# Kernel tuning notes

Hardware: AMD Instinct MI355X
Metric: run time of the kernel (lower is better)

The kernel has to match this reference:

```python
import jax, jax.numpy as jnp
import numpy as np
from jax import lax

D_MODEL = 1024
D_INNER = 2 * D_MODEL          # expand=2
D_STATE = 16
D_CONV = 4
DT_RANK = 64                   # ceil(1024/16)
DT_MIN = 0.001
DT_MAX = 0.1
BATCH = 4
SEQ = 2048


def setup_inputs() -> dict:
    key = jax.random.key(0)
    ks = jax.random.split(key, 8)
    s = lambda fan_in: 1.0 / np.sqrt(fan_in)
    x = jax.random.normal(ks[0], (BATCH, SEQ, D_MODEL), dtype=jnp.float32)
    # Linear weights stored as (in, out) so y = x @ W
    W_in = jax.random.uniform(ks[1], (D_MODEL, 2 * D_INNER), jnp.float32, -s(D_MODEL), s(D_MODEL))
    conv_w = jax.random.uniform(ks[2], (D_INNER, 1, D_CONV), jnp.float32, -s(D_CONV), s(D_CONV))
    conv_b = jax.random.uniform(ks[3], (D_INNER,), jnp.float32, -s(D_CONV), s(D_CONV))
    W_x = jax.random.uniform(ks[4], (D_INNER, DT_RANK + 2 * D_STATE), jnp.float32, -s(D_INNER), s(D_INNER))
    W_dt = jax.random.uniform(ks[5], (DT_RANK, D_INNER), jnp.float32, -s(DT_RANK), s(DT_RANK))
    b_dt = jax.random.uniform(ks[6], (D_INNER,), jnp.float32, -s(DT_RANK), s(DT_RANK))
    # A = arange(1..d_state) repeated over d_inner; store log(A)
    A_log = jnp.log(jnp.broadcast_to(jnp.arange(1, D_STATE + 1, dtype=jnp.float32), (D_INNER, D_STATE)))
    D_param = jnp.ones((D_INNER,), dtype=jnp.float32)
    W_out = jax.random.uniform(ks[7], (D_INNER, D_MODEL), jnp.float32, -s(D_INNER), s(D_INNER))
    return {"x": x, "W_in": W_in, "conv_w": conv_w, "conv_b": conv_b,
            "W_x": W_x, "W_dt": W_dt, "b_dt": b_dt, "A_log": A_log,
            "D_param": D_param, "W_out": W_out}


def reference(x, W_in, conv_w, conv_b, W_x, W_dt, b_dt, A_log, D_param, W_out):
    # in_proj + split
    xz = x @ W_in                                   # (B, S, 2*d_inner)
    x_branch, z_branch = jnp.split(xz, 2, axis=-1)  # each (B, S, d_inner)

    # causal depthwise conv1d (torch pads d_conv-1 both sides then slices [:seq])
    xc = jnp.pad(x_branch.transpose(0, 2, 1), ((0, 0), (0, 0), (D_CONV - 1, 0)))
    xc = lax.conv_general_dilated(xc, conv_w, (1,), 'VALID',
                                  dimension_numbers=('NCH', 'OIH', 'NCH'),
                                  feature_group_count=D_INNER)
    xc = xc + conv_b[None, :, None]
    x_conv = jax.nn.silu(xc.transpose(0, 2, 1))     # (B, S, d_inner)

    # input-dependent dt, B, C
    x_dbl = x_conv @ W_x                            # (B, S, dt_rank + 2*d_state)
    dt_low = x_dbl[..., :DT_RANK]
    Bm = x_dbl[..., DT_RANK:DT_RANK + D_STATE]      # (B, S, d_state)
    Cm = x_dbl[..., DT_RANK + D_STATE:]             # (B, S, d_state)
    dt = jax.nn.sigmoid(dt_low @ W_dt + b_dt) * (DT_MAX - DT_MIN) + DT_MIN
    dt = jnp.maximum(dt, 1e-4)                      # (B, S, d_inner)

    A = -jnp.exp(A_log)                             # (d_inner, d_state)

    # selective scan over time (n_substeps = 1)
    def step(h, inp):
        dt_t, B_t, C_t, x_t = inp                   # (B,di), (B,ds), (B,ds), (B,di)
        dA = jnp.exp(dt_t[:, :, None] * A[None])    # (B, di, ds)
        h = dA * h + (dt_t * x_t)[:, :, None] * B_t[:, None, :]
        y_t = jnp.sum(h * C_t[:, None, :], axis=-1) # (B, di)
        return h, y_t

    h0 = jnp.zeros((x.shape[0], D_INNER, D_STATE), dtype=x.dtype)
    _, ys = lax.scan(step, h0,
                     (dt.swapaxes(0, 1), Bm.swapaxes(0, 1),
                      Cm.swapaxes(0, 1), x_conv.swapaxes(0, 1)))
    y = ys.swapaxes(0, 1)                           # (B, S, d_inner)

    y = y + x_conv * D_param
    y = y * jax.nn.silu(z_branch)
    return y @ W_out                                # (B, S, d_model)
```

## Files before the change

kernel.cpp:

```cpp
#include <hip/hip_runtime.h>

typedef unsigned short u16;
typedef unsigned int u32;
typedef __attribute__((ext_vector_type(8))) short short8;
typedef __attribute__((ext_vector_type(4))) float f32x4;

#define NBATCH 4
#define NSEQ   2048
#define DMODEL 1024
#define DINNER 2048
#define DSTATE 16
#define DTRANK 64
#define ROWS   (NBATCH*NSEQ)
#define NCH    64
#define CLEN   32

__device__ __forceinline__ float b2f(u16 u){ union{u32 i; float f;} v; v.i=((u32)u)<<16; return v.f; }
__device__ __forceinline__ u16 f2b(float f){ union{float f; u32 i;} v; v.f=f; u32 i=v.i; return (u16)((i + 0x7FFFu + ((i>>16)&1u))>>16); }
__device__ __forceinline__ float sigmoidf_(float x){ return 1.0f/(1.0f+__expf(-x)); }

__global__ __launch_bounds__(256) void prep(const u16* __restrict__ x,
    const u16* __restrict__ Win, const u16* __restrict__ convw,
    const u16* __restrict__ Wx, const u16* __restrict__ Wdt,
    const u16* __restrict__ Alog, const u16* __restrict__ Wout,
    const u16* __restrict__ v0, const u16* __restrict__ v1, const u16* __restrict__ v2,
    int* __restrict__ meta){
  __shared__ int vote;
  __shared__ int mxbits;
  const int tid = threadIdx.x;
  const u16* V[3] = {v0, v1, v2};

  const u16* ptrs[6] = {x, Win, convw, Wx, Wdt, Wout};
  const float bounds[6] = {8.f, 0.045f, 0.6f, 0.035f, 0.15f, 0.035f};
  const int slots[6] = {0, 1, 2, 4, 5, 9};
  for (int q = 0; q < 6; q++){
    if (tid == 0) vote = 1;
    __syncthreads();
    int bad = 0;
    for (int i = tid; i < 2048; i += 256){
      float v = fabsf(b2f(ptrs[q][i]));
      if (!(v <= bounds[q])) bad = 1;
    }
    if (bad) atomicAnd(&vote, 0);
    __syncthreads();
    if (tid == 0) meta[slots[q]] = vote;
    __syncthreads();
  }
  if (tid == 0){ u16 u = Alog[1]; meta[7] = (u == 0x3F31 || u == 0x3F32) ? 1 : 0; }

  int iD = -1, fD = 1;
  for (int k = 0; k < 3; k++){
    if (V[k][0] == 0x3F80 && V[k][1] == 0x3F80){ iD = k; fD = 1; }
    else if (V[k][0] == 0 && V[k][1] == 0x3F80 && V[k][2] == 0){ iD = k; fD = 0; }
  }
  if (iD < 0){ iD = 2; fD = 1; }
  int oo[2], no = 0;
  for (int k = 0; k < 3; k++) if (k != iD) oo[no++] = k;
  int fo[2]; float mo[2];
  for (int q = 0; q < 2; q++){
    if (tid == 0) vote = 1;
    __syncthreads();
    int bad = 0;
    for (int i = tid; i < 2048; i += 256){
      float v = fabsf(b2f(V[oo[q]][i]));
      if (!(v <= 0.6f)) bad = 1;
    }
    if (bad) atomicAnd(&vote, 0);
    __syncthreads();
    fo[q] = vote;
    if (tid == 0) mxbits = 0;
    __syncthreads();
    float m = 0.f;
    for (int i = tid; i < 2048; i += 256){
      float v = fabsf(fo[q] ? b2f(V[oo[q]][i]) : ((const float*)V[oo[q]])[i]);
      m = fmaxf(m, v);
    }
    atomicMax(&mxbits, __float_as_int(m));
    __syncthreads();
    mo[q] = __int_as_float(mxbits);
    __syncthreads();
  }
  if (tid == 0){
    int a = (mo[0] > 0.25f) ? 0 : 1;
    meta[10] = oo[a];     meta[3] = fo[a];
    meta[11] = oo[1-a];   meta[6] = fo[1-a];
    meta[12] = iD;        meta[8] = fD;
  }
}

__global__ __launch_bounds__(256) void cvt_bf16(const void* __restrict__ in,
                                                u16* __restrict__ out, long n,
                                                const int* __restrict__ meta, int slot){
  long i = (long)blockIdx.x*256 + threadIdx.x;
  if (i >= n) return;
  if (meta[slot]) out[i] = ((const u16*)in)[i];
  else            out[i] = f2b(((const float*)in)[i]);
}

__global__ __launch_bounds__(256) void cvt_trio(const void* __restrict__ v0,
                                                const void* __restrict__ v1,
                                                const void* __restrict__ v2,
                                                const int* __restrict__ meta,
                                                u16* __restrict__ cbc,
                                                u16* __restrict__ bdtc,
                                                u16* __restrict__ dpc){
  int i = blockIdx.x*256 + threadIdx.x;
  int which = i >> 11, d = i & 2047;
  const void* V[3] = {v0, v1, v2};
  int src, fl; u16* dst;
  if (which == 0){ src = meta[10]; fl = meta[3]; dst = cbc; }
  else if (which == 1){ src = meta[11]; fl = meta[6]; dst = bdtc; }
  else { src = meta[12]; fl = meta[8]; dst = dpc; }
  dst[d] = fl ? ((const u16*)V[src])[d] : f2b(((const float*)V[src])[d]);
}

__global__ __launch_bounds__(256) void transpose_pad(const void* __restrict__ inv,
                                                     u16* __restrict__ out,
                                                     int K, int N, int Nout,
                                                     const int* __restrict__ meta, int slot){
  __shared__ u16 t[32][33];
  const int f = meta[slot];
  const u16*   ib = (const u16*)inv;
  const float* iff = (const float*)inv;
  int k0 = blockIdx.x*32, n0 = blockIdx.y*32;
  int tx = threadIdx.x & 31, ty = threadIdx.x >> 5;
  #pragma unroll
  for (int i=0;i<32;i+=8){
    int k = k0+ty+i, n = n0+tx;
    u16 v = 0;
    if (k<K && n<N) v = f ? ib[(long)k*N+n] : f2b(iff[(long)k*N+n]);
    t[ty+i][tx] = v;
  }
  __syncthreads();
  #pragma unroll
  for (int i=0;i<32;i+=8){
    int n = n0+ty+i, k = k0+tx;
    if (n<Nout && k<K) out[(long)n*K+k] = t[tx][ty+i];
  }
}

template<int MODE>
__global__ __launch_bounds__(256) void gemm_bt(
    const u16* __restrict__ A, int lda,
    const u16* __restrict__ Bt, int K,
    u16* __restrict__ C0, u16* __restrict__ C1, int ldc,
    const u16* __restrict__ bias, float* __restrict__ Cf)
{
  __shared__ u16 sa[128*64];
  __shared__ u16 sb[128*64];
  const int tid = threadIdx.x;
  const int lane = tid & 63;
  const int wave = tid >> 6;
  const int wm = (wave >> 1) * 64;
  const int wn = (wave & 1) * 64;
  const int lane15 = lane & 15;
  const int quad = lane >> 4;
  const long rowBase = (long)blockIdx.y * 128;
  const long colBase = (long)blockIdx.x * 128;

  f32x4 acc[4][4];
  #pragma unroll
  for (int i=0;i<4;i++)
    #pragma unroll
    for (int j=0;j<4;j++)
      #pragma unroll
      for (int r=0;r<4;r++) acc[i][j][r]=0.0f;

  const int e  = tid*8;
  const int r0 = e >> 6;
  const int c0 = e & 63;

  for (int kb=0; kb<K; kb+=64) {
    #pragma unroll
    for (int i=0;i<4;i++){
      const u16* ga = A + (rowBase + r0 + i*32)*lda + kb + c0;
      __builtin_amdgcn_global_load_lds((const __attribute__((address_space(1))) void*)ga,
                                       (__attribute__((address_space(3))) void*)&sa[e + i*2048],
                                       16, 0, 0);
    }
    #pragma unroll
    for (int i=0;i<4;i++){
      const u16* gb = Bt + (colBase + r0 + i*32)*(long)K + kb + c0;
      __builtin_amdgcn_global_load_lds((const __attribute__((address_space(1))) void*)gb,
                                       (__attribute__((address_space(3))) void*)&sb[e + i*2048],
                                       16, 0, 0);
    }
    __syncthreads();
    #pragma unroll
    for (int ko=0; ko<2; ko++){
      const int kk = ko*32 + quad*8;
      short8 af[4], bfr[4];
      #pragma unroll
      for (int i=0;i<4;i++) af[i]  = *(const short8*)&sa[(wm + i*16 + lane15)*64 + kk];
      #pragma unroll
      for (int j=0;j<4;j++) bfr[j] = *(const short8*)&sb[(wn + j*16 + lane15)*64 + kk];
      #pragma unroll
      for (int i=0;i<4;i++)
        #pragma unroll
        for (int j=0;j<4;j++)
          acc[i][j] = __builtin_amdgcn_mfma_f32_16x16x32_bf16(af[i], bfr[j], acc[i][j], 0, 0, 0);
    }
    __syncthreads();
  }

  #pragma unroll
  for (int i=0;i<4;i++){
    #pragma unroll
    for (int j=0;j<4;j++){
      long row = rowBase + wm + i*16 + quad*4;
      long col = colBase + wn + j*16 + lane15;
      #pragma unroll
      for (int r=0;r<4;r++){
        float v = acc[i][j][r];
        long rr = row + r;
        if (MODE == 0) {
          C0[rr*ldc + col] = f2b(v);
        } else if (MODE == 2) {
          float t  = sigmoidf_(v + b2f(bias[col]));
          float dv = fmaxf(t*0.099f + 0.001f, 1e-4f);
          C0[rr*ldc + col] = f2b(dv);
        } else if (MODE == 3) {
          Cf[rr*ldc + col] = v;
        }
      }
    }
  }
}

template<int MODE>
__global__ __launch_bounds__(512, 2) void gemm256(
    const u16* __restrict__ A, int lda,
    const u16* __restrict__ Bt, int K,
    u16* __restrict__ C0, u16* __restrict__ C1, int ldc,
    float* __restrict__ Cf)
{
  __shared__ u16 sa[2*16384];
  __shared__ u16 sb[2*16384];
  const int tid  = threadIdx.x;
  const int lane = tid & 63;
  const int wm   = (tid >> 6) >> 2;
  const int wn   = (tid >> 6) & 3;
  const int lane15 = lane & 15;
  const int quad   = lane >> 4;

  const int nwg  = gridDim.x * gridDim.y;
  const int orig = blockIdx.y * gridDim.x + blockIdx.x;
  const int swz  = (orig & 7) * (nwg >> 3) + (orig >> 3);
  const int bx   = swz % gridDim.x;
  const int by   = swz / gridDim.x;
  const long rowBase = (long)by * 256;
  const long colBase = (long)bx * 256;

  const int xorv = (lane15 & 7) << 3;
  const int k0   = (quad*8) ^ xorv;
  const int k1   = (32 + quad*8) ^ xorv;
  const int aBase = (wm*128 + lane15) * 64;
  const int bBase = (wn*64  + lane15) * 64;

  const int scol = ((tid & 7) ^ ((tid >> 3) & 7)) << 3;
  const int arow = tid >> 3;
  const int bsub = ((tid >> 8) & 1)*64 + ((tid & 255) >> 3);
  const int bdst = (tid & 7) * 8;

  f32x4 acc[8][4];
  #pragma unroll
  for (int i=0;i<8;i++)
    #pragma unroll
    for (int j=0;j<4;j++)
      #pragma unroll
      for (int r=0;r<4;r++) acc[i][j][r]=0.0f;

  const int nt = K >> 6;

  auto stageA = [&](int buf, int rs, int kb){
    const u16* g = A + (rowBase + rs + arow)*(long)lda + kb + scol;
    __builtin_amdgcn_global_load_lds((const __attribute__((address_space(1))) void*)g,
        (__attribute__((address_space(3))) void*)&sa[buf*16384 + rs*64 + tid*8], 16, 0, 0);
  };
  auto stageB = [&](int buf, int cq, int part, int kb){
    const int row = part*128 + cq*32 + bsub;
    const u16* g = Bt + (colBase + row)*(long)K + kb + scol;
    __builtin_amdgcn_global_load_lds((const __attribute__((address_space(1))) void*)g,
        (__attribute__((address_space(3))) void*)&sb[buf*16384 + row*64 + bdst], 16, 0, 0);
  };

  stageA(0,   0, 0); stageA(0, 128, 0);
  stageB(0, 0, 0, 0); stageB(0, 0, 1, 0);
  stageA(0,  64, 0); stageA(0, 192, 0);
  stageB(0, 1, 0, 0); stageB(0, 1, 1, 0);
  asm volatile("s_waitcnt vmcnt(4)\n\ts_barrier" ::: "memory");

  for (int t = 0; t < nt; ++t){
    const int cur = t & 1, nb = cur ^ 1;
    const int kb2 = (t+1) << 6;
    const bool pf = (t+1 < nt);
    const u16* sA = &sa[cur*16384];
    const u16* sB = &sb[cur*16384];
    short8 a0[4][2], a1[4][2], b0[2][2], b1[2][2];

    #pragma unroll
    for (int i=0;i<4;i++){
      a0[i][0] = *(const short8*)&sA[aBase + i*1024 + k0];
      a0[i][1] = *(const short8*)&sA[aBase + i*1024 + k1];
    }
    #pragma unroll
    for (int j=0;j<2;j++){
      b0[j][0] = *(const short8*)&sB[bBase + j*1024 + k0];
      b0[j][1] = *(const short8*)&sB[bBase + j*1024 + k1];
    }
    if (pf){ stageA(nb, 0, kb2); stageA(nb, 128, kb2); }
    __builtin_amdgcn_s_setprio(1);
    #pragma unroll
    for (int s=0;s<2;s++)
      #pragma unroll
      for (int i=0;i<4;i++)
        #pragma unroll
        for (int j=0;j<2;j++)
          acc[i][j] = __builtin_amdgcn_mfma_f32_16x16x32_bf16(a0[i][s], b0[j][s], acc[i][j], 0, 0, 0);
    __builtin_amdgcn_s_setprio(0);
    asm volatile("s_waitcnt vmcnt(4)\n\ts_barrier" ::: "memory");

    #pragma unroll
    for (int i=0;i<4;i++){
      a1[i][0] = *(const short8*)&sA[aBase + 4096 + i*1024 + k0];
      a1[i][1] = *(const short8*)&sA[aBase + 4096 + i*1024 + k1];
    }
    if (pf){ stageB(nb, 0, 0, kb2); stageB(nb, 0, 1, kb2); }
    __builtin_amdgcn_s_setprio(1);
    #pragma unroll
    for (int s=0;s<2;s++)
      #pragma unroll
      for (int i=0;i<4;i++)
        #pragma unroll
        for (int j=0;j<2;j++)
          acc[4+i][j] = __builtin_amdgcn_mfma_f32_16x16x32_bf16(a1[i][s], b0[j][s], acc[4+i][j], 0, 0, 0);
    __builtin_amdgcn_s_setprio(0);
    asm volatile("s_waitcnt vmcnt(4)\n\ts_barrier" ::: "memory");

    #pragma unroll
    for (int j=0;j<2;j++){
      b1[j][0] = *(const short8*)&sB[bBase + 2048 + j*1024 + k0];
      b1[j][1] = *(const short8*)&sB[bBase + 2048 + j*1024 + k1];
    }
    if (pf){ stageA(nb, 64, kb2); stageA(nb, 192, kb2); }
    __builtin_amdgcn_s_setprio(1);
    #pragma unroll
    for (int s=0;s<2;s++)
      #pragma unroll
      for (int i=0;i<4;i++)
        #pragma unroll
        for (int j=0;j<2;j++)
          acc[i][2+j] = __builtin_amdgcn_mfma_f32_16x16x32_bf16(a0[i][s], b1[j][s], acc[i][2+j], 0, 0, 0);
    __builtin_amdgcn_s_setprio(0);
    asm volatile("s_barrier" ::: "memory");

    if (pf){ stageB(nb, 1, 0, kb2); stageB(nb, 1, 1, kb2); }
    __builtin_amdgcn_s_setprio(1);
    #pragma unroll
    for (int s=0;s<2;s++)
      #pragma unroll
      for (int i=0;i<4;i++)
        #pragma unroll
        for (int j=0;j<2;j++)
          acc[4+i][2+j] = __builtin_amdgcn_mfma_f32_16x16x32_bf16(a1[i][s], b1[j][s], acc[4+i][2+j], 0, 0, 0);
    __builtin_amdgcn_s_setprio(0);
    asm volatile("s_waitcnt vmcnt(4)\n\ts_barrier" ::: "memory");
  }

  #pragma unroll
  for (int i=0;i<8;i++){
    const long row = rowBase + wm*128 + i*16 + quad*4;
    #pragma unroll
    for (int j=0;j<4;j++){
      const long col = colBase + wn*64 + j*16 + lane15;
      #pragma unroll
      for (int r=0;r<4;r++){
        const float v = acc[i][j][r];
        const long rr = row + r;
        if (MODE == 1){
          if (col < 2048) C0[rr*2048 + col] = f2b(v);
          else            C1[rr*2048 + (col-2048)] = f2b(v);
        } else {
          Cf[rr*ldc + col] = v;
        }
      }
    }
  }
}

__global__ __launch_bounds__(256) void conv_silu(const u16* __restrict__ xb,
                                                 const u16* __restrict__ w,
                                                 const u16* __restrict__ bias,
                                                 u16* __restrict__ xc){
  long idx8 = ((long)blockIdx.x*256 + threadIdx.x) * 8;
  int d = (int)(idx8 & (DINNER-1));
  int s = (int)((idx8 >> 11) & (NSEQ-1));
  int b = (int)(idx8 >> 22);

  short8 bv = *(const short8*)(bias + d);
  short8 wv0 = *(const short8*)(w + d*4);
  short8 wv1 = *(const short8*)(w + d*4 + 8);
  short8 wv2 = *(const short8*)(w + d*4 + 16);
  short8 wv3 = *(const short8*)(w + d*4 + 24);
  u16 wl[32];
  #pragma unroll
  for (int q=0;q<8;q++){ wl[q] = ((u16*)&wv0)[q]; wl[8+q] = ((u16*)&wv1)[q];
                         wl[16+q] = ((u16*)&wv2)[q]; wl[24+q] = ((u16*)&wv3)[q]; }

  float acc[8];
  #pragma unroll
  for (int l=0;l<8;l++) acc[l] = b2f(((u16*)&bv)[l]);

  #pragma unroll
  for (int j=0;j<4;j++){
    int t = s - 3 + j;
    if (t >= 0){
      short8 xv = *(const short8*)(xb + ((long)(b*NSEQ + t))*DINNER + d);
      #pragma unroll
      for (int l=0;l<8;l++)
        acc[l] += b2f(((u16*)&xv)[l]) * b2f(wl[l*4 + j]);
    }
  }
  short8 ov;
  #pragma unroll
  for (int l=0;l<8;l++){ float y = acc[l]*sigmoidf_(acc[l]); ((u16*)&ov)[l] = f2b(y); }
  *(short8*)(xc + idx8) = ov;
}

__global__ __launch_bounds__(256) void scan_pass1(const u16* __restrict__ dt,
                                                  const u16* __restrict__ xc,
                                                  const u16* __restrict__ xdbl,
                                                  const u16* __restrict__ Alog,
                                                  float* __restrict__ hend,
                                                  float* __restrict__ sumdt){
  int d = blockIdx.x*256 + threadIdx.x;
  int c = blockIdx.y;
  int b = blockIdx.z;
  __shared__ float sB[CLEN][DSTATE];
  for (int i=threadIdx.x; i<CLEN*DSTATE; i+=256){
    int t = i >> 4, s = i & 15;
    sB[t][s] = b2f(xdbl[((long)(b*NSEQ + c*CLEN + t))*128 + DTRANK + s]);
  }
  float Acf[DSTATE];
  bool fast = true;
  #pragma unroll
  for (int s=0;s<DSTATE;s++){
    Acf[s] = -__expf(b2f(Alog[d*DSTATE + s]));
    fast = fast && (fabsf(Acf[s] + (float)(s+1)) < 0.03f*(float)(s+1));
  }
  __syncthreads();

  float h[DSTATE];
  #pragma unroll
  for (int s=0;s<DSTATE;s++) h[s] = 0.0f;
  float sd = 0.0f;
  long base = ((long)(b*NSEQ + c*CLEN))*DINNER + d;
  float dtv = b2f(dt[base]);
  float xv  = b2f(xc[base]);
  if (fast){
    for (int t=0;t<CLEN;t++){
      long nxt = base + (long)((t+1<CLEN)?(t+1):t)*DINNER;
      float dtn = b2f(dt[nxt]);
      float xn  = b2f(xc[nxt]);
      float B[DSTATE];
      *(f32x4*)&B[0]  = *(const f32x4*)&sB[t][0];
      *(f32x4*)&B[4]  = *(const f32x4*)&sB[t][4];
      *(f32x4*)&B[8]  = *(const f32x4*)&sB[t][8];
      *(f32x4*)&B[12] = *(const f32x4*)&sB[t][12];
      float u = dtv*xv;
      sd += dtv;
      float e1 = __expf(-dtv);
      float p = e1;
      #pragma unroll
      for (int s=0;s<DSTATE;s++){
        h[s] = fmaf(p, h[s], u*B[s]);
        p *= e1;
      }
      dtv = dtn; xv = xn;
    }
  } else {
    for (int t=0;t<CLEN;t++){
      long nxt = base + (long)((t+1<CLEN)?(t+1):t)*DINNER;
      float dtn = b2f(dt[nxt]);
      float xn  = b2f(xc[nxt]);
      float B[DSTATE];
      *(f32x4*)&B[0]  = *(const f32x4*)&sB[t][0];
      *(f32x4*)&B[4]  = *(const f32x4*)&sB[t][4];
      *(f32x4*)&B[8]  = *(const f32x4*)&sB[t][8];
      *(f32x4*)&B[12] = *(const f32x4*)&sB[t][12];
      float u = dtv*xv;
      sd += dtv;
      #pragma unroll
      for (int s=0;s<DSTATE;s++){
        float dA = __expf(dtv * Acf[s]);
        h[s] = fmaf(dA, h[s], u*B[s]);
      }
      dtv = dtn; xv = xn;
    }
  }
  long hidx = ((long)(b*DINNER + d)*NCH + c)*DSTATE;
  #pragma unroll
  for (int s=0;s<DSTATE;s++) hend[hidx + s] = h[s];
  sumdt[(long)(b*DINNER + d)*NCH + c] = sd;
}

__global__ __launch_bounds__(256) void scan_pass2(float* __restrict__ hend,
                                                  const float* __restrict__ sumdt,
                                                  const u16* __restrict__ Alog){
  long i = (long)blockIdx.x*256 + threadIdx.x;
  int s = (int)(i & 15);
  long bd = i >> 4;
  int d = (int)(bd & (DINNER-1));
  float A = -__expf(b2f(Alog[d*DSTATE + s]));
  float run = 0.0f;
  long base = bd*NCH*DSTATE + s;
  for (int c=0;c<NCH;c++){
    float e = hend[base + (long)c*DSTATE];
    float decay = __expf(A * sumdt[bd*NCH + c]);
    hend[base + (long)c*DSTATE] = run;
    run = run*decay + e;
  }
}

__global__ __launch_bounds__(256) void scan_pass3(const u16* __restrict__ dt,
                                                  u16* __restrict__ xc,
                                                  const u16* __restrict__ zb,
                                                  const u16* __restrict__ xdbl,
                                                  const u16* __restrict__ Alog,
                                                  const u16* __restrict__ Dp,
                                                  const float* __restrict__ hstart){
  int d = blockIdx.x*256 + threadIdx.x;
  int c = blockIdx.y;
  int b = blockIdx.z;
  __shared__ float sB[CLEN][DSTATE];
  __shared__ float sC[CLEN][DSTATE];
  for (int i=threadIdx.x; i<CLEN*DSTATE; i+=256){
    int t = i >> 4, s = i & 15;
    long rb = ((long)(b*NSEQ + c*CLEN + t))*128;
    sB[t][s] = b2f(xdbl[rb + DTRANK + s]);
    sC[t][s] = b2f(xdbl[rb + DTRANK + DSTATE + s]);
  }
  float Acf[DSTATE];
  bool fast = true;
  #pragma unroll
  for (int s=0;s<DSTATE;s++){
    Acf[s] = -__expf(b2f(Alog[d*DSTATE + s]));
    fast = fast && (fabsf(Acf[s] + (float)(s+1)) < 0.03f*(float)(s+1));
  }
  __syncthreads();

  float h[DSTATE];
  long hidx = ((long)(b*DINNER + d)*NCH + c)*DSTATE;
  #pragma unroll
  for (int s=0;s<DSTATE;s++) h[s] = hstart[hidx + s];
  float Dpv = b2f(Dp[d]);
  long base = ((long)(b*NSEQ + c*CLEN))*DINNER + d;
  float dtv = b2f(dt[base]);
  float xv  = b2f(xc[base]);
  float zv  = b2f(zb[base]);
  if (fast){
    for (int t=0;t<CLEN;t++){
      long nxt = base + (long)((t+1<CLEN)?(t+1):t)*DINNER;
      float dtn = b2f(dt[nxt]);
      float xn  = b2f(xc[nxt]);
      float zn  = b2f(zb[nxt]);
      float B[DSTATE], C[DSTATE];
      *(f32x4*)&B[0]  = *(const f32x4*)&sB[t][0];
      *(f32x4*)&B[4]  = *(const f32x4*)&sB[t][4];
      *(f32x4*)&B[8]  = *(const f32x4*)&sB[t][8];
      *(f32x4*)&B[12] = *(const f32x4*)&sB[t][12];
      *(f32x4*)&C[0]  = *(const f32x4*)&sC[t][0];
      *(f32x4*)&C[4]  = *(const f32x4*)&sC[t][4];
      *(f32x4*)&C[8]  = *(const f32x4*)&sC[t][8];
      *(f32x4*)&C[12] = *(const f32x4*)&sC[t][12];
      float u = dtv*xv;
      float e1 = __expf(-dtv);
      float gate = zv*sigmoidf_(zv);
      float p = e1;
      float y = 0.0f;
      #pragma unroll
      for (int s=0;s<DSTATE;s++){
        h[s] = fmaf(p, h[s], u*B[s]);
        y = fmaf(h[s], C[s], y);
        p *= e1;
      }
      y = fmaf(xv, Dpv, y);
      y *= gate;
      xc[base + (long)t*DINNER] = f2b(y);
      dtv = dtn; xv = xn; zv = zn;
    }
  } else {
    for (int t=0;t<CLEN;t++){
      long nxt = base + (long)((t+1<CLEN)?(t+1):t)*DINNER;
      float dtn = b2f(dt[nxt]);
      float xn  = b2f(xc[nxt]);
      float zn  = b2f(zb[nxt]);
      float B[DSTATE], C[DSTATE];
      *(f32x4*)&B[0]  = *(const f32x4*)&sB[t][0];
      *(f32x4*)&B[4]  = *(const f32x4*)&sB[t][4];
      *(f32x4*)&B[8]  = *(const f32x4*)&sB[t][8];
      *(f32x4*)&B[12] = *(const f32x4*)&sB[t][12];
      *(f32x4*)&C[0]  = *(const f32x4*)&sC[t][0];
      *(f32x4*)&C[4]  = *(const f32x4*)&sC[t][4];
      *(f32x4*)&C[8]  = *(const f32x4*)&sC[t][8];
      *(f32x4*)&C[12] = *(const f32x4*)&sC[t][12];
      float u = dtv*xv;
      float gate = zv*sigmoidf_(zv);
      float y = 0.0f;
      #pragma unroll
      for (int s=0;s<DSTATE;s++){
        float dA = __expf(dtv * Acf[s]);
        h[s] = fmaf(dA, h[s], u*B[s]);
        y = fmaf(h[s], C[s], y);
      }
      y = fmaf(xv, Dpv, y);
      y *= gate;
      xc[base + (long)t*DINNER] = f2b(y);
      dtv = dtn; xv = xn; zv = zn;
    }
  }
}

extern "C" void kernel_launch(void* const* d_in, const int* in_sizes, int n_in,
                              void* d_out, int out_size, void* d_ws, size_t ws_size,
                              hipStream_t stream) {
  const void *x=nullptr,*W_in=nullptr,*conv_w=nullptr,*W_x=nullptr,*W_dt=nullptr,
             *A_log=nullptr,*W_out=nullptr;
  const void* v2048[3] = {nullptr,nullptr,nullptr};
  int n2048 = 0;
  for (int i = 0; i < n_in; i++){
    switch (in_sizes[i]){
      case 8388608: x      = d_in[i]; break;
      case 4194304: W_in   = d_in[i]; break;
      case 8192:    conv_w = d_in[i]; break;
      case 196608:  W_x    = d_in[i]; break;
      case 131072:  W_dt   = d_in[i]; break;
      case 32768:   A_log  = d_in[i]; break;
      case 2097152: W_out  = d_in[i]; break;
      case 2048:    if (n2048 < 3) v2048[n2048++] = d_in[i]; break;
      default: break;
    }
  }

  size_t off = 0;
  char* wsb = (char*)d_ws;
  auto take = [&](size_t n){ void* p = wsb + off; off += (n + 255) & ~(size_t)255; return p; };
  u16* Wt_in  = (u16*)take((size_t)4096*1024*2);
  u16* Wt_x   = (u16*)take((size_t)128*2048*2);
  u16* Wt_dt  = (u16*)take((size_t)2048*64*2);
  u16* Wt_out = (u16*)take((size_t)1024*2048*2);
  u16* xb     = (u16*)take((size_t)ROWS*DINNER*2);
  u16* zb     = (u16*)take((size_t)ROWS*DINNER*2);
  u16* xc     = (u16*)take((size_t)ROWS*DINNER*2);
  u16* xdbl   = (u16*)take((size_t)ROWS*128*2);
  char* shr = (char*)take((size_t)ROWS*NCH*DSTATE*4 + (size_t)ROWS*NCH*4 + 4096);
  u16*   xcvt  = (u16*)shr;
  float* hend  = (float*)shr;
  float* sumdt = (float*)(shr + (size_t)ROWS*NCH*DSTATE*4);
  u16* cwc  = (u16*)take(DINNER*4*2);
  u16* cbc  = (u16*)take(DINNER*2);
  u16* bdtc = (u16*)take(DINNER*2);
  u16* alc  = (u16*)take(DINNER*DSTATE*2);
  u16* dpc  = (u16*)take(DINNER*2);
  int* meta = (int*)take(256);
  u16* dtb = xb;

  prep<<<1, 256, 0, stream>>>((const u16*)x, (const u16*)W_in, (const u16*)conv_w,
                              (const u16*)W_x, (const u16*)W_dt, (const u16*)A_log,
                              (const u16*)W_out,
                              (const u16*)v2048[0], (const u16*)v2048[1], (const u16*)v2048[2],
                              meta);

  cvt_bf16<<<(ROWS*DMODEL)/256, 256, 0, stream>>>(x, xcvt, (long)ROWS*DMODEL, meta, 0);
  cvt_bf16<<<32, 256, 0, stream>>>(conv_w, cwc, DINNER*4, meta, 2);
  cvt_bf16<<<128,256, 0, stream>>>(A_log, alc, DINNER*DSTATE, meta, 7);
  cvt_trio<<<24, 256, 0, stream>>>(v2048[0], v2048[1], v2048[2], meta, cbc, bdtc, dpc);

  transpose_pad<<<dim3(32,128), 256, 0, stream>>>(W_in, Wt_in, 1024, 4096, 4096, meta, 1);
  transpose_pad<<<dim3(64,4),   256, 0, stream>>>(W_x,  Wt_x,  2048, 96,   128,  meta, 4);
  transpose_pad<<<dim3(2,64),   256, 0, stream>>>(W_dt, Wt_dt, 64,   2048, 2048, meta, 5);
  transpose_pad<<<dim3(64,32),  256, 0, stream>>>(W_out,Wt_out,2048, 1024, 1024, meta, 9);

  gemm256<1><<<dim3(16,32), 512, 0, stream>>>(xcvt, 1024, Wt_in, 1024, xb, zb, 2048, nullptr);

  conv_silu<<<(ROWS*DINNER)/(256*8), 256, 0, stream>>>(xb, cwc, cbc, xc);

  gemm_bt<0><<<dim3(1,64), 256, 0, stream>>>(xc, 2048, Wt_x, 2048, xdbl, nullptr, 128, nullptr, nullptr);

  gemm_bt<2><<<dim3(16,64), 256, 0, stream>>>(xdbl, 128, Wt_dt, 64, dtb, nullptr, 2048, bdtc, nullptr);

  scan_pass1<<<dim3(8,NCH,NBATCH), 256, 0, stream>>>(dtb, xc, xdbl, alc, hend, sumdt);
  scan_pass2<<<(ROWS*DSTATE)/256, 256, 0, stream>>>(hend, sumdt, alc);
  scan_pass3<<<dim3(8,NCH,NBATCH), 256, 0, stream>>>(dtb, xc, zb, xdbl, alc, dpc, hend);

  gemm_bt<3><<<dim3(8,64), 256, 0, stream>>>(xc, 2048, Wt_out, 2048, nullptr, nullptr, 1024, nullptr, (float*)d_out);
}
```

Measured before the change: 476.4 us.

## Split-K the x_proj GEMM, vectorize x conversion, 4 channels per scan thread

```diff
diff --git a/kernel.cpp b/kernel.cpp
--- a/kernel.cpp
+++ b/kernel.cpp
@@ -3,6 +3,7 @@
 typedef unsigned short u16;
 typedef unsigned int u32;
 typedef __attribute__((ext_vector_type(8))) short short8;
+typedef __attribute__((ext_vector_type(4))) short short4v;
 typedef __attribute__((ext_vector_type(4))) float f32x4;
 
 #define NBATCH 4
@@ -95,6 +96,23 @@
   if (i >= n) return;
   if (meta[slot]) out[i] = ((const u16*)in)[i];
   else            out[i] = f2b(((const float*)in)[i]);
+}
+
+__global__ __launch_bounds__(256) void cvt_x8(const void* __restrict__ in,
+                                              u16* __restrict__ out,
+                                              const int* __restrict__ meta){
+  long i8 = ((long)blockIdx.x*256 + threadIdx.x)*8;
+  if (meta[0]){
+    *(short8*)(out + i8) = *(const short8*)((const u16*)in + i8);
+  } else {
+    const float* f = (const float*)in + i8;
+    f32x4 a = *(const f32x4*)f;
+    f32x4 b = *(const f32x4*)(f+4);
+    short8 o;
+    #pragma unroll
+    for (int j=0;j<4;j++){ ((u16*)&o)[j] = f2b(a[j]); ((u16*)&o)[4+j] = f2b(b[j]); }
+    *(short8*)(out + i8) = o;
+  }
 }
 
 __global__ __launch_bounds__(256) void cvt_trio(const void* __restrict__ v0,
@@ -158,6 +176,14 @@
   const long rowBase = (long)blockIdx.y * 128;
   const long colBase = (long)blockIdx.x * 128;
 
+  int kbeg = 0, kend = K;
+  if (MODE == 4){
+    const int span = K >> 2;
+    kbeg = blockIdx.z * span;
+    kend = kbeg + span;
+    Cf += (long)blockIdx.z * (8192L*128);
+  }
+
   f32x4 acc[4][4];
   #pragma unroll
   for (int i=0;i<4;i++)
@@ -170,7 +196,7 @@
   const int r0 = e >> 6;
   const int c0 = e & 63;
 
-  for (int kb=0; kb<K; kb+=64) {
+  for (int kb=kbeg; kb<kend; kb+=64) {
     #pragma unroll
     for (int i=0;i<4;i++){
       const u16* ga = A + (rowBase + r0 + i*32)*lda + kb + c0;
@@ -219,12 +245,25 @@
           float t  = sigmoidf_(v + b2f(bias[col]));
           float dv = fmaxf(t*0.099f + 0.001f, 1e-4f);
           C0[rr*ldc + col] = f2b(dv);
-        } else if (MODE == 3) {
+        } else if (MODE == 3 || MODE == 4) {
           Cf[rr*ldc + col] = v;
         }
       }
     }
   }
+}
+
+__global__ __launch_bounds__(256) void reduce_xdbl(const float* __restrict__ P,
+                                                   u16* __restrict__ out){
+  const long i4 = ((long)blockIdx.x*256 + threadIdx.x)*4;
+  f32x4 a = *(const f32x4*)(P + i4);
+  f32x4 b = *(const f32x4*)(P + 1048576 + i4);
+  f32x4 c = *(const f32x4*)(P + 2097152 + i4);
+  f32x4 d = *(const f32x4*)(P + 3145728 + i4);
+  short4v o;
+  #pragma unroll
+  for (int j=0;j<4;j++) ((u16*)&o)[j] = f2b(a[j]+b[j]+c[j]+d[j]);
+  *(short4v*)(out + i4) = o;
 }
 
 template<int MODE>
@@ -433,75 +472,97 @@
                                                   const u16* __restrict__ Alog,
                                                   float* __restrict__ hend,
                                                   float* __restrict__ sumdt){
-  int d = blockIdx.x*256 + threadIdx.x;
-  int c = blockIdx.y;
-  int b = blockIdx.z;
+  const int tid = threadIdx.x;
+  const int d0 = blockIdx.x*1024 + tid*4;
+  const int c = blockIdx.y;
+  const int b = blockIdx.z;
   __shared__ float sB[CLEN][DSTATE];
-  for (int i=threadIdx.x; i<CLEN*DSTATE; i+=256){
+  for (int i=tid; i<CLEN*DSTATE; i+=256){
     int t = i >> 4, s = i & 15;
     sB[t][s] = b2f(xdbl[((long)(b*NSEQ + c*CLEN + t))*128 + DTRANK + s]);
   }
-  float Acf[DSTATE];
   bool fast = true;
   #pragma unroll
-  for (int s=0;s<DSTATE;s++){
-    Acf[s] = -__expf(b2f(Alog[d*DSTATE + s]));
-    fast = fast && (fabsf(Acf[s] + (float)(s+1)) < 0.03f*(float)(s+1));
-  }
+  for (int j=0;j<4;j++)
+    #pragma unroll
+    for (int s=0;s<DSTATE;s++){
+      float a = -__expf(b2f(Alog[(d0+j)*DSTATE + s]));
+      fast = fast && (fabsf(a + (float)(s+1)) < 0.03f*(float)(s+1));
+    }
   __syncthreads();
 
-  float h[DSTATE];
-  #pragma unroll
-  for (int s=0;s<DSTATE;s++) h[s] = 0.0f;
-  float sd = 0.0f;
-  long base = ((long)(b*NSEQ + c*CLEN))*DINNER + d;
-  float dtv = b2f(dt[base]);
-  float xv  = b2f(xc[base]);
+  float h[4][DSTATE];
+  #pragma unroll
+  for (int j=0;j<4;j++)
+    #pragma unroll
+    for (int s=0;s<DSTATE;s++) h[j][s] = 0.0f;
+  float sd[4] = {0.f,0.f,0.f,0.f};
+  long base = ((long)(b*NSEQ + c*CLEN))*DINNER + d0;
+  short4v dt4 = *(const short4v*)(dt + base);
+  short4v x4  = *(const short4v*)(xc + base);
   if (fast){
     for (int t=0;t<CLEN;t++){
       long nxt = base + (long)((t+1<CLEN)?(t+1):t)*DINNER;
-      float dtn = b2f(dt[nxt]);
-      float xn  = b2f(xc[nxt]);
+      short4v dtn = *(const short4v*)(dt + nxt);
+      short4v xn  = *(const short4v*)(xc + nxt);
       float B[DSTATE];
       *(f32x4*)&B[0]  = *(const f32x4*)&sB[t][0];
       *(f32x4*)&B[4]  = *(const f32x4*)&sB[t][4];
       *(f32x4*)&B[8]  = *(const f32x4*)&sB[t][8];
       *(f32x4*)&B[12] = *(const f32x4*)&sB[t][12];
-      float u = dtv*xv;
-      sd += dtv;
-      float e1 = __expf(-dtv);
-      float p = e1;
-      #pragma unroll
-      for (int s=0;s<DSTATE;s++){
-        h[s] = fmaf(p, h[s], u*B[s]);
-        p *= e1;
+      #pragma unroll
+      for (int j=0;j<4;j++){
+        float dtv = b2f(((u16*)&dt4)[j]);
+        float xv  = b2f(((u16*)&x4)[j]);
+        float u = dtv*xv;
+        sd[j] += dtv;
+        float e1 = __expf(-dtv);
+        float p = e1;
+        #pragma unroll
+        for (int s=0;s<DSTATE;s++){
+          h[j][s] = fmaf(p, h[j][s], u*B[s]);
+          p *= e1;
+        }
       }
-      dtv = dtn; xv = xn;
+      dt4 = dtn; x4 = xn;
     }
   } else {
+    float Acf[4][DSTATE];
+    #pragma unroll
+    for (int j=0;j<4;j++)
+      #pragma unroll
+      for (int s=0;s<DSTATE;s++) Acf[j][s] = -__expf(b2f(Alog[(d0+j)*DSTATE + s]));
     for (int t=0;t<CLEN;t++){
       long nxt = base + (long)((t+1<CLEN)?(t+1):t)*DINNER;
-      float dtn = b2f(dt[nxt]);
-      float xn  = b2f(xc[nxt]);
+      short4v dtn = *(const short4v*)(dt + nxt);
+      short4v xn  = *(const short4v*)(xc + nxt);
       float B[DSTATE];
       *(f32x4*)&B[0]  = *(const f32x4*)&sB[t][0];
       *(f32x4*)&B[4]  = *(const f32x4*)&sB[t][4];
       *(f32x4*)&B[8]  = *(const f32x4*)&sB[t][8];
       *(f32x4*)&B[12] = *(const f32x4*)&sB[t][12];
-      float u = dtv*xv;
-      sd += dtv;
-      #pragma unroll
-      for (int s=0;s<DSTATE;s++){
-        float dA = __expf(dtv * Acf[s]);
-        h[s] = fmaf(dA, h[s], u*B[s]);
+      #pragma unroll
+      for (int j=0;j<4;j++){
+        float dtv = b2f(((u16*)&dt4)[j]);
+        float xv  = b2f(((u16*)&x4)[j]);
+        float u = dtv*xv;
+        sd[j] += dtv;
+        #pragma unroll
+        for (int s=0;s<DSTATE;s++){
+          float dA = __expf(dtv * Acf[j][s]);
+          h[j][s] = fmaf(dA, h[j][s], u*B[s]);
+        }
       }
-      dtv = dtn; xv = xn;
-    }
-  }
-  long hidx = ((long)(b*DINNER + d)*NCH + c)*DSTATE;
-  #pragma unroll
-  for (int s=0;s<DSTATE;s++) hend[hidx + s] = h[s];
-  sumdt[(long)(b*DINNER + d)*NCH + c] = sd;
+      dt4 = dtn; x4 = xn;
+    }
+  }
+  #pragma unroll
+  for (int j=0;j<4;j++){
+    long hidx = ((long)(b*DINNER + d0 + j)*NCH + c)*DSTATE;
+    #pragma unroll
+    for (int q=0;q<4;q++) *(f32x4*)&hend[hidx + q*4] = *(const f32x4*)&h[j][q*4];
+    sumdt[(long)(b*DINNER + d0 + j)*NCH + c] = sd[j];
+  }
 }
 
 __global__ __launch_bounds__(256) void scan_pass2(float* __restrict__ hend,
@@ -529,41 +590,46 @@
                                                   const u16* __restrict__ Alog,
                                                   const u16* __restrict__ Dp,
                                                   const float* __restrict__ hstart){
-  int d = blockIdx.x*256 + threadIdx.x;
-  int c = blockIdx.y;
-  int b = blockIdx.z;
+  const int tid = threadIdx.x;
+  const int d0 = blockIdx.x*1024 + tid*4;
+  const int c = blockIdx.y;
+  const int b = blockIdx.z;
   __shared__ float sB[CLEN][DSTATE];
   __shared__ float sC[CLEN][DSTATE];
-  for (int i=threadIdx.x; i<CLEN*DSTATE; i+=256){
+  for (int i=tid; i<CLEN*DSTATE; i+=256){
     int t = i >> 4, s = i & 15;
     long rb = ((long)(b*NSEQ + c*CLEN + t))*128;
     sB[t][s] = b2f(xdbl[rb + DTRANK + s]);
     sC[t][s] = b2f(xdbl[rb + DTRANK + DSTATE + s]);
   }
-  float Acf[DSTATE];
   bool fast = true;
   #pragma unroll
-  for (int s=0;s<DSTATE;s++){
-    Acf[s] = -__expf(b2f(Alog[d*DSTATE + s]));
-    fast = fast && (fabsf(Acf[s] + (float)(s+1)) < 0.03f*(float)(s+1));
-  }
+  for (int j=0;j<4;j++)
+    #pragma unroll
+    for (int s=0;s<DSTATE;s++){
+      float a = -__expf(b2f(Alog[(d0+j)*DSTATE + s]));
+      fast = fast && (fabsf(a + (float)(s+1)) < 0.03f*(float)(s+1));
+    }
   __syncthreads();
 
-  float h[DSTATE];
-  long hidx = ((long)(b*DINNER + d)*NCH + c)*DSTATE;
-  #pragma unroll
-  for (int s=0;s<DSTATE;s++) h[s] = hstart[hidx + s];
-  float Dpv = b2f(Dp[d]);
-  long base = ((long)(b*NSEQ + c*CLEN))*DINNER + d;
-  float dtv = b2f(dt[base]);
-  float xv  = b2f(xc[base]);
-  float zv  = b2f(zb[base]);
+  float h[4][DSTATE];
+  #pragma unroll
+  for (int j=0;j<4;j++){
+    long hidx = ((long)(b*DINNER + d0 + j)*NCH + c)*DSTATE;
+    #pragma unroll
+    for (int q=0;q<4;q++) *(f32x4*)&h[j][q*4] = *(const f32x4*)&hstart[hidx + q*4];
+  }
+  short4v dp4 = *(const short4v*)(Dp + d0);
+  long base = ((long)(b*NSEQ + c*CLEN))*DINNER + d0;
+  short4v dt4 = *(const short4v*)(dt + base);
+  short4v x4  = *(const short4v*)(xc + base);
+  short4v z4  = *(const short4v*)(zb + base);
   if (fast){
     for (int t=0;t<CLEN;t++){
       long nxt = base + (long)((t+1<CLEN)?(t+1):t)*DINNER;
-      float dtn = b2f(dt[nxt]);
-      float xn  = b2f(xc[nxt]);
-      float zn  = b2f(zb[nxt]);
+      short4v dtn = *(const short4v*)(dt + nxt);
+      short4v xn  = *(const short4v*)(xc + nxt);
+      short4v zn  = *(const short4v*)(zb + nxt);
       float B[DSTATE], C[DSTATE];
       *(f32x4*)&B[0]  = *(const f32x4*)&sB[t][0];
       *(f32x4*)&B[4]  = *(const f32x4*)&sB[t][4];
@@ -573,28 +639,41 @@
       *(f32x4*)&C[4]  = *(const f32x4*)&sC[t][4];
       *(f32x4*)&C[8]  = *(const f32x4*)&sC[t][8];
       *(f32x4*)&C[12] = *(const f32x4*)&sC[t][12];
-      float u = dtv*xv;
-      float e1 = __expf(-dtv);
-      float gate = zv*sigmoidf_(zv);
-      float p = e1;
-      float y = 0.0f;
-      #pragma unroll
-      for (int s=0;s<DSTATE;s++){
-        h[s] = fmaf(p, h[s], u*B[s]);
-        y = fmaf(h[s], C[s], y);
-        p *= e1;
+      short4v ov;
+      #pragma unroll
+      for (int j=0;j<4;j++){
+        float dtv = b2f(((u16*)&dt4)[j]);
+        float xv  = b2f(((u16*)&x4)[j]);
+        float zv  = b2f(((u16*)&z4)[j]);
+        float u = dtv*xv;
+        float e1 = __expf(-dtv);
+        float gate = zv*sigmoidf_(zv);
+        float p = e1;
+        float y = 0.0f;
+        #pragma unroll
+        for (int s=0;s<DSTATE;s++){
+          h[j][s] = fmaf(p, h[j][s], u*B[s]);
+          y = fmaf(h[j][s], C[s], y);
+          p *= e1;
+        }
+        y = fmaf(xv, b2f(((u16*)&dp4)[j]), y);
+        y *= gate;
+        ((u16*)&ov)[j] = f2b(y);
       }
-      y = fmaf(xv, Dpv, y);
-      y *= gate;
-      xc[base + (long)t*DINNER] = f2b(y);
-      dtv = dtn; xv = xn; zv = zn;
+      *(short4v*)(xc + base + (long)t*DINNER) = ov;
+      dt4 = dtn; x4 = xn; z4 = zn;
     }
   } else {
+    float Acf[4][DSTATE];
+    #pragma unroll
+    for (int j=0;j<4;j++)
+      #pragma unroll
+      for (int s=0;s<DSTATE;s++) Acf[j][s] = -__expf(b2f(Alog[(d0+j)*DSTATE + s]));
     for (int t=0;t<CLEN;t++){
       long nxt = base + (long)((t+1<CLEN)?(t+1):t)*DINNER;
-      float dtn = b2f(dt[nxt]);
-      float xn  = b2f(xc[nxt]);
-      float zn  = b2f(zb[nxt]);
+      short4v dtn = *(const short4v*)(dt + nxt);
+      short4v xn  = *(const short4v*)(xc + nxt);
+      short4v zn  = *(const short4v*)(zb + nxt);
       float B[DSTATE], C[DSTATE];
       *(f32x4*)&B[0]  = *(const f32x4*)&sB[t][0];
       *(f32x4*)&B[4]  = *(const f32x4*)&sB[t][4];
@@ -604,19 +683,27 @@
       *(f32x4*)&C[4]  = *(const f32x4*)&sC[t][4];
       *(f32x4*)&C[8]  = *(const f32x4*)&sC[t][8];
       *(f32x4*)&C[12] = *(const f32x4*)&sC[t][12];
-      float u = dtv*xv;
-      float gate = zv*sigmoidf_(zv);
-      float y = 0.0f;
-      #pragma unroll
-      for (int s=0;s<DSTATE;s++){
-        float dA = __expf(dtv * Acf[s]);
-        h[s] = fmaf(dA, h[s], u*B[s]);
-        y = fmaf(h[s], C[s], y);
+      short4v ov;
+      #pragma unroll
+      for (int j=0;j<4;j++){
+        float dtv = b2f(((u16*)&dt4)[j]);
+        float xv  = b2f(((u16*)&x4)[j]);
+        float zv  = b2f(((u16*)&z4)[j]);
+        float u = dtv*xv;
+        float gate = zv*sigmoidf_(zv);
+        float y = 0.0f;
+        #pragma unroll
+        for (int s=0;s<DSTATE;s++){
+          float dA = __expf(dtv * Acf[j][s]);
+          h[j][s] = fmaf(dA, h[j][s], u*B[s]);
+          y = fmaf(h[j][s], C[s], y);
+        }
+        y = fmaf(xv, b2f(((u16*)&dp4)[j]), y);
+        y *= gate;
+        ((u16*)&ov)[j] = f2b(y);
       }
-      y = fmaf(xv, Dpv, y);
-      y *= gate;
-      xc[base + (long)t*DINNER] = f2b(y);
-      dtv = dtn; xv = xn; zv = zn;
+      *(short4v*)(xc + base + (long)t*DINNER) = ov;
+      dt4 = dtn; x4 = xn; z4 = zn;
     }
   }
 }
@@ -663,6 +750,7 @@
   u16* alc  = (u16*)take(DINNER*DSTATE*2);
   u16* dpc  = (u16*)take(DINNER*2);
   int* meta = (int*)take(256);
+  float* xdp = (float*)take((size_t)4*8192*128*4);
   u16* dtb = xb;
 
   prep<<<1, 256, 0, stream>>>((const u16*)x, (const u16*)W_in, (const u16*)conv_w,
@@ -671,7 +759,7 @@
                               (const u16*)v2048[0], (const u16*)v2048[1], (const u16*)v2048[2],
                               meta);
 
-  cvt_bf16<<<(ROWS*DMODEL)/256, 256, 0, stream>>>(x, xcvt, (long)ROWS*DMODEL, meta, 0);
+  cvt_x8<<<(ROWS*DMODEL)/(256*8), 256, 0, stream>>>(x, xcvt, meta);
   cvt_bf16<<<32, 256, 0, stream>>>(conv_w, cwc, DINNER*4, meta, 2);
   cvt_bf16<<<128,256, 0, stream>>>(A_log, alc, DINNER*DSTATE, meta, 7);
   cvt_trio<<<24, 256, 0, stream>>>(v2048[0], v2048[1], v2048[2], meta, cbc, bdtc, dpc);
@@ -685,13 +773,14 @@
 
   conv_silu<<<(ROWS*DINNER)/(256*8), 256, 0, stream>>>(xb, cwc, cbc, xc);
 
-  gemm_bt<0><<<dim3(1,64), 256, 0, stream>>>(xc, 2048, Wt_x, 2048, xdbl, nullptr, 128, nullptr, nullptr);
+  gemm_bt<4><<<dim3(1,64,4), 256, 0, stream>>>(xc, 2048, Wt_x, 2048, nullptr, nullptr, 128, nullptr, xdp);
+  reduce_xdbl<<<1024, 256, 0, stream>>>(xdp, xdbl);
 
   gemm_bt<2><<<dim3(16,64), 256, 0, stream>>>(xdbl, 128, Wt_dt, 64, dtb, nullptr, 2048, bdtc, nullptr);
 
-  scan_pass1<<<dim3(8,NCH,NBATCH), 256, 0, stream>>>(dtb, xc, xdbl, alc, hend, sumdt);
+  scan_pass1<<<dim3(2,NCH,NBATCH), 256, 0, stream>>>(dtb, xc, xdbl, alc, hend, sumdt);
   scan_pass2<<<(ROWS*DSTATE)/256, 256, 0, stream>>>(hend, sumdt, alc);
-  scan_pass3<<<dim3(8,NCH,NBATCH), 256, 0, stream>>>(dtb, xc, zb, xdbl, alc, dpc, hend);
+  scan_pass3<<<dim3(2,NCH,NBATCH), 256, 0, stream>>>(dtb, xc, zb, xdbl, alc, dpc, hend);
 
   gemm_bt<3><<<dim3(8,64), 256, 0, stream>>>(xc, 2048, Wt_out, 2048, nullptr, nullptr, 1024, nullptr, (float*)d_out);
 }
```

Result: no change. 470.8 us (-1.2%).
